# Performance work log

Measured on AMD Instinct MI355X. Metric: run time of the kernel, lower is better.

The kernel has to match this reference:

```python
import jax, jax.numpy as jnp
import numpy as np

N_NODES = 50000
N_EDGES = 800000
IN_CH, HID_CH, OUT_CH = 512, 256, 128


def setup_inputs() -> dict:
    key = jax.random.key(0)
    k = jax.random.split(key, 6)
    x = jax.random.normal(k[0], (N_NODES, IN_CH), dtype=jnp.float32)
    edge_index = jax.random.randint(k[1], (2, N_EDGES), 0, N_NODES, dtype=jnp.int64)
    # Glorot-ish scaled weights
    W0 = jax.random.normal(k[2], (IN_CH, HID_CH), dtype=jnp.float32) * (1.0 / np.sqrt(IN_CH))
    b0 = jnp.zeros((HID_CH,), dtype=jnp.float32)
    W1 = jax.random.normal(k[3], (HID_CH, OUT_CH), dtype=jnp.float32) * (1.0 / np.sqrt(HID_CH))
    b1 = jnp.zeros((OUT_CH,), dtype=jnp.float32)
    PW = jax.random.normal(k[4], (OUT_CH, OUT_CH), dtype=jnp.float32) * (1.0 / np.sqrt(OUT_CH))
    Pb = jnp.zeros((OUT_CH,), dtype=jnp.float32)
    return {"x": x, "edge_index": edge_index, "W0": W0, "b0": b0,
            "W1": W1, "b1": b1, "PW": PW, "Pb": Pb}


def reference(x, edge_index, W0, b0, W1, b1, PW, Pb):
    N = x.shape[0]
    # GCN normalization with added self-loops (edge_weight=None -> ones)
    loop = jnp.arange(N, dtype=edge_index.dtype)
    src = jnp.concatenate([edge_index[0], loop])  # [E+N]
    dst = jnp.concatenate([edge_index[1], loop])
    w = jnp.ones(src.shape[0], dtype=x.dtype)
    deg = jax.ops.segment_sum(w, dst, num_segments=N)  # in-degree incl. self-loop
    dinv = jnp.where(deg > 0, jax.lax.rsqrt(jnp.maximum(deg, 1e-12)), 0.0)
    norm = dinv[src] * dinv[dst]  # [E+N]

    def gcn_conv(h, W, b):
        hl = h @ W                               # [N, F_out] linear first (PyG GCNConv)
        msg = norm[:, None] * hl[src]            # gather + scale  [E+N, F_out]
        return jax.ops.segment_sum(msg, dst, num_segments=N) + b

    # eval mode: dropout is identity
    h = jax.nn.relu(gcn_conv(x, W0, b0))
    h = gcn_conv(h, W1, b1)                      # last layer: no relu
    p = h @ PW + Pb                              # PGE linear [N, OUT]
    vals = jnp.max(p, axis=0)                    # torch.max(dim=0) -> (values, indices)
    idx = jnp.argmax(p, axis=0)
    return (h, vals, idx)
```

## Files before the change

### kernel.cpp

```cpp
#include <hip/hip_runtime.h>
#include <stdint.h>

#define N_NODES 50000
#define N_EDGES 800000
#define IN_CH   512
#define HID_CH  256
#define OUT_CH  128
#define NPAD    50048
#define SLOT    96

#define NB_E   3125
#define NB2    391
#define AP     36

#define PBKT  NB_E
#define PW0B  (PBKT + 64)
#define PW1B  (PW0B + 16)
#define PPWB  (PW1B + 8)

typedef unsigned short ushort_t;
typedef __attribute__((ext_vector_type(8))) short    short8;
typedef __attribute__((ext_vector_type(4))) float    floatx4;
typedef __attribute__((ext_vector_type(4))) _Float16 half4v;
typedef __attribute__((ext_vector_type(2))) _Float16 half2v;

__device__ inline ushort_t f2bf(float x) {
    union { float f; unsigned u; } v; v.f = x;
    unsigned r = v.u + 0x7fffu + ((v.u >> 16) & 1u);
    return (ushort_t)(r >> 16);
}
__device__ inline float bf2f(ushort_t h) {
    union { unsigned u; float f; } v; v.u = ((unsigned)h) << 16;
    return v.f;
}
__device__ inline void gl_lds16(const void* g, void* l) {
    __builtin_amdgcn_global_load_lds((const __attribute__((address_space(1))) void*)g,
                                     (__attribute__((address_space(3))) void*)l, 16, 0, 0);
}

#define SWZ(r) ((((r) >> 1) & 3) << 3)

__device__ inline void conv_splitT8(const float* __restrict__ W,
                                    ushort_t* __restrict__ WhT,
                                    ushort_t* __restrict__ WlT,
                                    int K, int N, int base) {
    float4 v0 = *(const float4*)(W + base);
    float4 v1 = *(const float4*)(W + base + 4);
    float vv[8] = {v0.x, v0.y, v0.z, v0.w, v1.x, v1.y, v1.z, v1.w};
    #pragma unroll
    for (int j = 0; j < 8; ++j) {
        int g = base + j;
        int k = g / N, n = g - k * N;
        int ks = k ^ SWZ(n);
        ushort_t h = f2bf(vv[j]);
        WhT[(size_t)n * K + ks] = h;
        WlT[(size_t)n * K + ks] = f2bf(vv[j] - bf2f(h));
    }
}

__global__ __launch_bounds__(256) void k_prep(const int* __restrict__ esrc,
                                              const int* __restrict__ edst,
                                              const float* __restrict__ W0,
                                              const float* __restrict__ W1,
                                              const float* __restrict__ PW,
                                              int* __restrict__ cnt,
                                              int* __restrict__ slots,
                                              ushort_t* W0hT, ushort_t* W0lT,
                                              ushort_t* W1hT, ushort_t* W1lT,
                                              ushort_t* PWhT, ushort_t* PWlT) {
    int b = blockIdx.x, tid = threadIdx.x;
    if (b < PBKT) {
        int e = b * 256 + tid;
        if (e < N_EDGES) {
            int d = edst[e];
            int c = atomicAdd(&cnt[d], 1);
            slots[(size_t)d * SLOT + c] = esrc[e];
        }
    } else if (b < PW0B) {
        conv_splitT8(W0, W0hT, W0lT, IN_CH, HID_CH, (b - PBKT) * 2048 + tid * 8);
    } else if (b < PW1B) {
        conv_splitT8(W1, W1hT, W1lT, HID_CH, OUT_CH, (b - PW0B) * 2048 + tid * 8);
    } else {
        conv_splitT8(PW, PWhT, PWlT, OUT_CH, OUT_CH, (b - PW1B) * 2048 + tid * 8);
    }
}

__global__ __launch_bounds__(256) void k_dinv(const int* __restrict__ cnt,
                                              float* __restrict__ dinv) {
    int i = blockIdx.x * 256 + threadIdx.x;
    if (i < N_NODES) dinv[i] = rsqrtf((float)cnt[i] + 1.0f);
}

__global__ __launch_bounds__(256, 3) void gemm0_x(const float* __restrict__ A,
                                                  const ushort_t* __restrict__ BhT,
                                                  const ushort_t* __restrict__ BlT,
                                                  const float* __restrict__ dinv,
                                                  _Float16* __restrict__ C,
                                                  int M, int N) {
    constexpr int KT = IN_CH;
    constexpr int NT = KT / 32;
    __shared__ float    smA[128 * AP];
    __shared__ ushort_t smB[2][128 * 32];
    const int tid  = threadIdx.x;
    const int wave = tid >> 6, lane = tid & 63;
    const int m0 = blockIdx.y * 128, n0 = blockIdx.x * 128;

    const float* psrc[5];
    float*       adst[5];
    #pragma unroll
    for (int i = 0; i < 5; ++i) {
        int c = wave + 4 * i;
        int cc = (c < 18) ? c : 0;
        int p = cc * 256 + lane * 4;
        int r = p / AP, col = p - r * AP;
        int gr = min(m0 + r, M - 1);
        int gc = (col < 32) ? col : 0;
        psrc[i] = A + (size_t)gr * KT + gc;
        adst[i] = smA + cc * 256;
    }

    const int c0 = wave * 128 + lane, c1 = c0 + 64;
    const ushort_t* gbh0 = BhT + (size_t)(n0 + (c0 >> 2)) * KT + (c0 & 3) * 8;
    const ushort_t* gbh1 = BhT + (size_t)(n0 + (c1 >> 2)) * KT + (c1 & 3) * 8;
    const ushort_t* gbl0 = BlT + (size_t)(n0 + (c0 >> 2)) * KT + (c0 & 3) * 8;
    const ushort_t* gbl1 = BlT + (size_t)(n0 + (c1 >> 2)) * KT + (c1 & 3) * 8;
    ushort_t* lb0 = &smB[0][wave * 1024];  ushort_t* lb1 = &smB[0][wave * 1024 + 512];
    ushort_t* lc0 = &smB[1][wave * 1024];  ushort_t* lc1 = &smB[1][wave * 1024 + 512];

    floatx4 zero = {0.f, 0.f, 0.f, 0.f};
    floatx4 acc[4][4];
    #pragma unroll
    for (int i = 0; i < 4; ++i)
        #pragma unroll
        for (int j = 0; j < 4; ++j) acc[i][j] = zero;

    const int wm = (wave & 1) * 64, wn = (wave >> 1) * 64;
    const int fr = lane & 15, fq = lane >> 4;
    const int sx = SWZ(fr);

    for (int t = 0; t < NT; ++t) {
        #pragma unroll
        for (int i = 0; i < 5; ++i)
            if (wave + 4 * i < 18) { gl_lds16(psrc[i], adst[i]); psrc[i] += 32; }
        gl_lds16(gbh0, lb0); gl_lds16(gbh1, lb1);
        gl_lds16(gbl0, lc0); gl_lds16(gbl1, lc1);
        gbh0 += 32; gbh1 += 32; gbl0 += 32; gbl1 += 32;
        __syncthreads();
        short8 afh[4], afl[4], bfh[4], bfl[4];
        #pragma unroll
        for (int tt = 0; tt < 4; ++tt) {
            const float* ap = &smA[(wm + tt * 16 + fr) * AP + fq * 8];
            float4 v0 = *(const float4*)ap;
            float4 v1 = *(const float4*)(ap + 4);
            float f[8] = {v0.x, v0.y, v0.z, v0.w, v1.x, v1.y, v1.z, v1.w};
            union { unsigned u[4]; short8 v; } hh, ll;
            #pragma unroll
            for (int j = 0; j < 4; ++j) {
                unsigned ua = __float_as_uint(f[2 * j]);
                unsigned ub = __float_as_uint(f[2 * j + 1]);
                unsigned ha = ua & 0xffff0000u, hb = ub & 0xffff0000u;
                hh.u[j] = (ha >> 16) | hb;
                float ra = f[2 * j]     - __uint_as_float(ha);
                float rb = f[2 * j + 1] - __uint_as_float(hb);
                ll.u[j] = (__float_as_uint(ra) >> 16) | (__float_as_uint(rb) & 0xffff0000u);
            }
            afh[tt] = hh.v; afl[tt] = ll.v;
            int bi = (wn + tt * 16 + fr) * 32 + (fq * 8 ^ sx);
            bfh[tt] = *(const short8*)&smB[0][bi];
            bfl[tt] = *(const short8*)&smB[1][bi];
        }
        #pragma unroll
        for (int i = 0; i < 4; ++i)
            #pragma unroll
            for (int j = 0; j < 4; ++j) {
                acc[i][j] = __builtin_amdgcn_mfma_f32_16x16x32_bf16(afh[i], bfh[j], acc[i][j], 0, 0, 0);
                acc[i][j] = __builtin_amdgcn_mfma_f32_16x16x32_bf16(afh[i], bfl[j], acc[i][j], 0, 0, 0);
                acc[i][j] = __builtin_amdgcn_mfma_f32_16x16x32_bf16(afl[i], bfh[j], acc[i][j], 0, 0, 0);
            }
        __syncthreads();
    }
    const int colb = n0 + wn + fr;
    #pragma unroll
    for (int i = 0; i < 4; ++i) {
        int rowb = m0 + wm + i * 16 + fq * 4;
        #pragma unroll
        for (int r = 0; r < 4; ++r) {
            int row = rowb + r;
            if (row < M) {
                float dv = dinv[row];
                _Float16* cp = C + (size_t)row * N + colb;
                cp[0]  = (_Float16)(acc[i][0][r] * dv);
                cp[16] = (_Float16)(acc[i][1][r] * dv);
                cp[32] = (_Float16)(acc[i][2][r] * dv);
                cp[48] = (_Float16)(acc[i][3][r] * dv);
            }
        }
    }
}

template <int KT>
__global__ __launch_bounds__(256) void gemm_bf(const ushort_t* __restrict__ Ah,
                                               const ushort_t* __restrict__ Al,
                                               const ushort_t* __restrict__ BhT,
                                               const ushort_t* __restrict__ BlT,
                                               const float* __restrict__ dinv,
                                               _Float16* __restrict__ C,
                                               int M, int N) {
    constexpr int NT = KT / 32;
    __shared__ ushort_t sm[4][128 * 32];
    const int tid  = threadIdx.x;
    const int wave = tid >> 6, lane = tid & 63;
    const int m0 = blockIdx.y * 128, n0 = blockIdx.x * 128;

    const int c0 = wave * 128 + lane, c1 = c0 + 64;
    const int ar0 = min(m0 + (c0 >> 2), M - 1), ar1 = min(m0 + (c1 >> 2), M - 1);
    const ushort_t* gah0 = Ah + (size_t)ar0 * KT + (c0 & 3) * 8;
    const ushort_t* gah1 = Ah + (size_t)ar1 * KT + (c1 & 3) * 8;
    const ushort_t* gal0 = Al + (size_t)ar0 * KT + (c0 & 3) * 8;
    const ushort_t* gal1 = Al + (size_t)ar1 * KT + (c1 & 3) * 8;
    const ushort_t* gbh0 = BhT + (size_t)(n0 + (c0 >> 2)) * KT + (c0 & 3) * 8;
    const ushort_t* gbh1 = BhT + (size_t)(n0 + (c1 >> 2)) * KT + (c1 & 3) * 8;
    const ushort_t* gbl0 = BlT + (size_t)(n0 + (c0 >> 2)) * KT + (c0 & 3) * 8;
    const ushort_t* gbl1 = BlT + (size_t)(n0 + (c1 >> 2)) * KT + (c1 & 3) * 8;
    ushort_t* la0 = &sm[0][wave * 1024];       ushort_t* la1 = &sm[0][wave * 1024 + 512];
    ushort_t* ll0 = &sm[1][wave * 1024];       ushort_t* ll1 = &sm[1][wave * 1024 + 512];
    ushort_t* lb0 = &sm[2][wave * 1024];       ushort_t* lb1 = &sm[2][wave * 1024 + 512];
    ushort_t* lc0 = &sm[3][wave * 1024];       ushort_t* lc1 = &sm[3][wave * 1024 + 512];

    floatx4 zero = {0.f, 0.f, 0.f, 0.f};
    floatx4 acc[4][4];
    #pragma unroll
    for (int i = 0; i < 4; ++i)
        #pragma unroll
        for (int j = 0; j < 4; ++j) acc[i][j] = zero;

    const int wm = (wave & 1) * 64, wn = (wave >> 1) * 64;
    const int fr = lane & 15, fq = lane >> 4;
    const int sx = SWZ(fr);

    for (int t = 0; t < NT; ++t) {
        gl_lds16(gah0, la0); gl_lds16(gah1, la1);
        gl_lds16(gal0, ll0); gl_lds16(gal1, ll1);
        gl_lds16(gbh0, lb0); gl_lds16(gbh1, lb1);
        gl_lds16(gbl0, lc0); gl_lds16(gbl1, lc1);
        gah0 += 32; gah1 += 32; gal0 += 32; gal1 += 32;
        gbh0 += 32; gbh1 += 32; gbl0 += 32; gbl1 += 32;
        __syncthreads();
        short8 afh[4], afl[4], bfh[4], bfl[4];
        #pragma unroll
        for (int tt = 0; tt < 4; ++tt) {
            int ai = (wm + tt * 16 + fr) * 32 + (fq * 8 ^ sx);
            int bi = (wn + tt * 16 + fr) * 32 + (fq * 8 ^ sx);
            afh[tt] = *(const short8*)&sm[0][ai];
            afl[tt] = *(const short8*)&sm[1][ai];
            bfh[tt] = *(const short8*)&sm[2][bi];
            bfl[tt] = *(const short8*)&sm[3][bi];
        }
        #pragma unroll
        for (int i = 0; i < 4; ++i)
            #pragma unroll
            for (int j = 0; j < 4; ++j) {
                acc[i][j] = __builtin_amdgcn_mfma_f32_16x16x32_bf16(afh[i], bfh[j], acc[i][j], 0, 0, 0);
                acc[i][j] = __builtin_amdgcn_mfma_f32_16x16x32_bf16(afh[i], bfl[j], acc[i][j], 0, 0, 0);
                acc[i][j] = __builtin_amdgcn_mfma_f32_16x16x32_bf16(afl[i], bfh[j], acc[i][j], 0, 0, 0);
            }
        __syncthreads();
    }
    const int colb = n0 + wn + fr;
    #pragma unroll
    for (int i = 0; i < 4; ++i) {
        int rowb = m0 + wm + i * 16 + fq * 4;
        #pragma unroll
        for (int r = 0; r < 4; ++r) {
            int row = rowb + r;
            if (row < M) {
                float dv = dinv[row];
                _Float16* cp = C + (size_t)row * N + colb;
                cp[0]  = (_Float16)(acc[i][0][r] * dv);
                cp[16] = (_Float16)(acc[i][1][r] * dv);
                cp[32] = (_Float16)(acc[i][2][r] * dv);
                cp[48] = (_Float16)(acc[i][3][r] * dv);
            }
        }
    }
}

__global__ __launch_bounds__(256) void gemm_pge(const ushort_t* __restrict__ Ah,
                                                const ushort_t* __restrict__ Al,
                                                const ushort_t* __restrict__ BhT,
                                                const ushort_t* __restrict__ BlT,
                                                float* __restrict__ pv,
                                                int* __restrict__ pi,
                                                int M) {
    constexpr int KT = OUT_CH;
    constexpr int NT = KT / 32;
    __shared__ ushort_t sm[4][128 * 32];
    __shared__ float redv[8][128];
    __shared__ int   redi[8][128];
    const int tid  = threadIdx.x;
    const int wave = tid >> 6, lane = tid & 63;
    const int m0 = blockIdx.x * 128;

    const int c0 = wave * 128 + lane, c1 = c0 + 64;
    const int ar0 = min(m0 + (c0 >> 2), M - 1), ar1 = min(m0 + (c1 >> 2), M - 1);
    const ushort_t* gah0 = Ah + (size_t)ar0 * KT + (c0 & 3) * 8;
    const ushort_t* gah1 = Ah + (size_t)ar1 * KT + (c1 & 3) * 8;
    const ushort_t* gal0 = Al + (size_t)ar0 * KT + (c0 & 3) * 8;
    const ushort_t* gal1 = Al + (size_t)ar1 * KT + (c1 & 3) * 8;
    const ushort_t* gbh0 = BhT + (size_t)(c0 >> 2) * KT + (c0 & 3) * 8;
    const ushort_t* gbh1 = BhT + (size_t)(c1 >> 2) * KT + (c1 & 3) * 8;
    const ushort_t* gbl0 = BlT + (size_t)(c0 >> 2) * KT + (c0 & 3) * 8;
    const ushort_t* gbl1 = BlT + (size_t)(c1 >> 2) * KT + (c1 & 3) * 8;
    ushort_t* la0 = &sm[0][wave * 1024];       ushort_t* la1 = &sm[0][wave * 1024 + 512];
    ushort_t* ll0 = &sm[1][wave * 1024];       ushort_t* ll1 = &sm[1][wave * 1024 + 512];
    ushort_t* lb0 = &sm[2][wave * 1024];       ushort_t* lb1 = &sm[2][wave * 1024 + 512];
    ushort_t* lc0 = &sm[3][wave * 1024];       ushort_t* lc1 = &sm[3][wave * 1024 + 512];

    floatx4 zero = {0.f, 0.f, 0.f, 0.f};
    floatx4 acc[4][4];
    #pragma unroll
    for (int i = 0; i < 4; ++i)
        #pragma unroll
        for (int j = 0; j < 4; ++j) acc[i][j] = zero;

    const int wm = (wave & 1) * 64, wn = (wave >> 1) * 64;
    const int fr = lane & 15, fq = lane >> 4;
    const int sx = SWZ(fr);

    for (int t = 0; t < NT; ++t) {
        gl_lds16(gah0, la0); gl_lds16(gah1, la1);
        gl_lds16(gal0, ll0); gl_lds16(gal1, ll1);
        gl_lds16(gbh0, lb0); gl_lds16(gbh1, lb1);
        gl_lds16(gbl0, lc0); gl_lds16(gbl1, lc1);
        gah0 += 32; gah1 += 32; gal0 += 32; gal1 += 32;
        gbh0 += 32; gbh1 += 32; gbl0 += 32; gbl1 += 32;
        __syncthreads();
        short8 afh[4], afl[4], bfh[4], bfl[4];
        #pragma unroll
        for (int tt = 0; tt < 4; ++tt) {
            int ai = (wm + tt * 16 + fr) * 32 + (fq * 8 ^ sx);
            int bi = (wn + tt * 16 + fr) * 32 + (fq * 8 ^ sx);
            afh[tt] = *(const short8*)&sm[0][ai];
            afl[tt] = *(const short8*)&sm[1][ai];
            bfh[tt] = *(const short8*)&sm[2][bi];
            bfl[tt] = *(const short8*)&sm[3][bi];
        }
        #pragma unroll
        for (int i = 0; i < 4; ++i)
            #pragma unroll
            for (int j = 0; j < 4; ++j) {
                acc[i][j] = __builtin_amdgcn_mfma_f32_16x16x32_bf16(afh[i], bfh[j], acc[i][j], 0, 0, 0);
                acc[i][j] = __builtin_amdgcn_mfma_f32_16x16x32_bf16(afh[i], bfl[j], acc[i][j], 0, 0, 0);
                acc[i][j] = __builtin_amdgcn_mfma_f32_16x16x32_bf16(afl[i], bfh[j], acc[i][j], 0, 0, 0);
            }
        __syncthreads();
    }
    const int slot = (wave & 1) * 4 + fq;
    #pragma unroll
    for (int j = 0; j < 4; ++j) {
        float bv = -3.402823466e+38f; int bidx = 0;
        #pragma unroll
        for (int i = 0; i < 4; ++i) {
            int rowb = m0 + wm + i * 16 + fq * 4;
            #pragma unroll
            for (int r = 0; r < 4; ++r) {
                int row = rowb + r;
                float v = acc[i][j][r];
                if (row < M && v > bv) { bv = v; bidx = row; }
            }
        }
        redv[slot][wn + j * 16 + fr] = bv;
        redi[slot][wn + j * 16 + fr] = bidx;
    }
    __syncthreads();
    if (tid < 128) {
        float bv = redv[0][tid]; int bidx = redi[0][tid];
        #pragma unroll
        for (int s = 1; s < 8; ++s) {
            float v = redv[s][tid]; int ix = redi[s][tid];
            if (v > bv || (v == bv && ix < bidx)) { bv = v; bidx = ix; }
        }
        pv[blockIdx.x * 128 + tid] = bv;
        pi[blockIdx.x * 128 + tid] = bidx;
    }
}

__global__ __launch_bounds__(128) void agg256_relu_bf(const _Float16* __restrict__ hl,
                                                      const float* __restrict__ dinv,
                                                      const int* __restrict__ cnt,
                                                      const int* __restrict__ slots,
                                                      const float* __restrict__ bias,
                                                      ushort_t* __restrict__ oh,
                                                      ushort_t* __restrict__ ol) {
    int d = blockIdx.x * 2 + (threadIdx.x >> 6);
    int lane = threadIdx.x & 63;
    float di = dinv[d];
    half4v v = ((const half4v*)(hl + (size_t)d * 256))[lane];
    float ax = (float)v[0], ay = (float)v[1], az = (float)v[2], aw = (float)v[3];
    const int* sl = slots + (size_t)d * SLOT;
    int n = cnt[d];
    for (int e = 0; e < n; e += 8) {
        int s[8]; float m[8]; half4v u[8];
        #pragma unroll
        for (int j = 0; j < 8; ++j) {
            bool live = (e + j) < n;
            s[j] = live ? sl[e + j] : d;
            m[j] = live ? 1.0f : 0.0f;
        }
        #pragma unroll
        for (int j = 0; j < 8; ++j) u[j] = ((const half4v*)(hl + (size_t)s[j] * 256))[lane];
        #pragma unroll
        for (int j = 0; j < 8; ++j) {
            ax += m[j] * (float)u[j][0]; ay += m[j] * (float)u[j][1];
            az += m[j] * (float)u[j][2]; aw += m[j] * (float)u[j][3];
        }
    }
    float4 b = ((const float4*)bias)[lane];
    float rx = fmaxf(fmaf(di, ax, b.x), 0.0f), ry = fmaxf(fmaf(di, ay, b.y), 0.0f);
    float rz = fmaxf(fmaf(di, az, b.z), 0.0f), rw = fmaxf(fmaf(di, aw, b.w), 0.0f);
    ushort4 hv, lv;
    hv.x = f2bf(rx); lv.x = f2bf(rx - bf2f(hv.x));
    hv.y = f2bf(ry); lv.y = f2bf(ry - bf2f(hv.y));
    hv.z = f2bf(rz); lv.z = f2bf(rz - bf2f(hv.z));
    hv.w = f2bf(rw); lv.w = f2bf(rw - bf2f(hv.w));
    int sidx = (lane * 4) ^ SWZ(d);
    *(ushort4*)&oh[(size_t)d * 256 + sidx] = hv;
    *(ushort4*)&ol[(size_t)d * 256 + sidx] = lv;
}

__global__ __launch_bounds__(128) void agg128_bias_bf(const _Float16* __restrict__ hl,
                                                      const float* __restrict__ dinv,
                                                      const int* __restrict__ cnt,
                                                      const int* __restrict__ slots,
                                                      const float* __restrict__ bias,
                                                      float* __restrict__ out,
                                                      ushort_t* __restrict__ oh,
                                                      ushort_t* __restrict__ ol) {
    int d = blockIdx.x * 2 + (threadIdx.x >> 6);
    int lane = threadIdx.x & 63;
    float di = dinv[d];
    half2v v = ((const half2v*)(hl + (size_t)d * 128))[lane];
    float ax = (float)v[0], ay = (float)v[1];
    const int* sl = slots + (size_t)d * SLOT;
    int n = cnt[d];
    for (int e = 0; e < n; e += 8) {
        int s[8]; float m[8]; half2v u[8];
        #pragma unroll
        for (int j = 0; j < 8; ++j) {
            bool live = (e + j) < n;
            s[j] = live ? sl[e + j] : d;
            m[j] = live ? 1.0f : 0.0f;
        }
        #pragma unroll
        for (int j = 0; j < 8; ++j) u[j] = ((const half2v*)(hl + (size_t)s[j] * 128))[lane];
        #pragma unroll
        for (int j = 0; j < 8; ++j) { ax += m[j] * (float)u[j][0]; ay += m[j] * (float)u[j][1]; }
    }
    float2 b = ((const float2*)bias)[lane];
    float rx = fmaf(di, ax, b.x), ry = fmaf(di, ay, b.y);
    ((float2*)(out + (size_t)d * 128))[lane] = make_float2(rx, ry);
    ushort2 hv, lv;
    hv.x = f2bf(rx); lv.x = f2bf(rx - bf2f(hv.x));
    hv.y = f2bf(ry); lv.y = f2bf(ry - bf2f(hv.y));
    int sidx = (lane * 2) ^ SWZ(d);
    *(ushort2*)&oh[(size_t)d * 128 + sidx] = hv;
    *(ushort2*)&ol[(size_t)d * 128 + sidx] = lv;
}

__global__ __launch_bounds__(256) void k_reduce2(const float* __restrict__ pv,
                                                 const int* __restrict__ pi,
                                                 const float* __restrict__ Pb,
                                                 float* __restrict__ out) {
    int c = threadIdx.x & 127, sub = threadIdx.x >> 7;
    float best = -3.402823466e+38f;
    int bi = 0;
    for (int b = sub; b < NB2; b += 2) {
        float v = pv[b * 128 + c];
        int ix = pi[b * 128 + c];
        if (v > best || (v == best && ix < bi)) { best = v; bi = ix; }
    }
    __shared__ float sv[128];
    __shared__ int   si[128];
    if (sub == 1) { sv[c] = best; si[c] = bi; }
    __syncthreads();
    if (sub == 0) {
        float v1 = sv[c]; int i1 = si[c];
        if (v1 > best || (v1 == best && i1 < bi)) { best = v1; bi = i1; }
        out[(size_t)N_NODES * OUT_CH + c]       = best + Pb[c];
        out[(size_t)N_NODES * OUT_CH + 128 + c] = (float)bi;
    }
}

extern "C" void kernel_launch(void* const* d_in, const int* in_sizes, int n_in,
                              void* d_out, int out_size, void* d_ws, size_t ws_size,
                              hipStream_t stream) {
    const float* x  = (const float*)d_in[0];
    const int*   ei = (const int*)d_in[1];
    const float* W0 = (const float*)d_in[2];
    const float* b0 = (const float*)d_in[3];
    const float* W1 = (const float*)d_in[4];
    const float* b1 = (const float*)d_in[5];
    const float* PW = (const float*)d_in[6];
    const float* Pb = (const float*)d_in[7];
    float* out = (float*)d_out;
    const int* esrc = ei;
    const int* edst = ei + N_EDGES;

    char* w = (char*)d_ws;
    size_t off = 0;
    auto alloc = [&](size_t bytes) -> void* {
        void* p = (void*)(w + off);
        off = (off + bytes + 255) & ~(size_t)255;
        return p;
    };
    int*       cnt    = (int*)alloc((size_t)N_NODES * 4);
    float*     dinv   = (float*)alloc((size_t)N_NODES * 4);
    int*       slots  = (int*)alloc((size_t)N_NODES * SLOT * 4);
    float*     pmax_v = (float*)alloc((size_t)NB2 * 128 * 4);
    int*       pmax_i = (int*)alloc((size_t)NB2 * 128 * 4);
    _Float16*  bufH   = (_Float16*)alloc((size_t)NPAD * 256 * 2);
    ushort_t*  h0h    = (ushort_t*)alloc((size_t)N_NODES * HID_CH * 2);
    ushort_t*  h0l    = (ushort_t*)alloc((size_t)N_NODES * HID_CH * 2);
    ushort_t*  h1h    = (ushort_t*)alloc((size_t)N_NODES * OUT_CH * 2);
    ushort_t*  h1l    = (ushort_t*)alloc((size_t)N_NODES * OUT_CH * 2);
    ushort_t*  W0hT   = (ushort_t*)alloc((size_t)IN_CH * HID_CH * 2);
    ushort_t*  W0lT   = (ushort_t*)alloc((size_t)IN_CH * HID_CH * 2);
    ushort_t*  W1hT   = (ushort_t*)alloc((size_t)HID_CH * OUT_CH * 2);
    ushort_t*  W1lT   = (ushort_t*)alloc((size_t)HID_CH * OUT_CH * 2);
    ushort_t*  PWhT   = (ushort_t*)alloc((size_t)OUT_CH * OUT_CH * 2);
    ushort_t*  PWlT   = (ushort_t*)alloc((size_t)OUT_CH * OUT_CH * 2);

    hipMemsetAsync(cnt, 0, (size_t)N_NODES * 4, stream);
    k_prep<<<PPWB, 256, 0, stream>>>(esrc, edst, W0, W1, PW, cnt, slots,
                                     W0hT, W0lT, W1hT, W1lT, PWhT, PWlT);
    k_dinv<<<196, 256, 0, stream>>>(cnt, dinv);

    gemm0_x<<<dim3(HID_CH / 128, NB2), 256, 0, stream>>>(
        x, W0hT, W0lT, dinv, bufH, N_NODES, HID_CH);
    agg256_relu_bf<<<N_NODES / 2, 128, 0, stream>>>(bufH, dinv, cnt, slots, b0, h0h, h0l);

    gemm_bf<HID_CH><<<dim3(1, NB2), 256, 0, stream>>>(
        h0h, h0l, W1hT, W1lT, dinv, bufH, N_NODES, OUT_CH);
    agg128_bias_bf<<<N_NODES / 2, 128, 0, stream>>>(bufH, dinv, cnt, slots, b1,
                                                    out, h1h, h1l);

    gemm_pge<<<NB2, 256, 0, stream>>>(h1h, h1l, PWhT, PWlT, pmax_v, pmax_i, N_NODES);
    k_reduce2<<<1, 256, 0, stream>>>(pmax_v, pmax_i, Pb, out);

    (void)in_sizes; (void)n_in; (void)out_size; (void)ws_size;
}
```

Measured before the change: 452.8 us.

## Convert A to split-bf16 once in LDS, prefetch next tile, inline dinv

The first GEMM now loads x tiles into registers, splits them into bf16 hi/lo once, and stores them swizzled in LDS. The next tile is prefetched during compute using explicit waitcnt and barriers, so each wave no longer redoes the conversion on its own LDS reads. The separate dinv kernel is removed and rsqrt(cnt+1) is computed inline in the GEMM epilogues and aggregation kernels. Aggregation gathers unroll to 16 and the GEMMs get an occupancy hint of 4. The hand-placed waitcnt counts are fragile and raise register pressure.

```diff
diff --git a/kernel.cpp b/kernel.cpp
--- a/kernel.cpp
+++ b/kernel.cpp
@@ -11,7 +11,6 @@
 
 #define NB_E   3125
 #define NB2    391
-#define AP     36
 
 #define PBKT  NB_E
 #define PW0B  (PBKT + 64)
@@ -85,39 +84,25 @@
     }
 }
 
-__global__ __launch_bounds__(256) void k_dinv(const int* __restrict__ cnt,
-                                              float* __restrict__ dinv) {
-    int i = blockIdx.x * 256 + threadIdx.x;
-    if (i < N_NODES) dinv[i] = rsqrtf((float)cnt[i] + 1.0f);
-}
-
-__global__ __launch_bounds__(256, 3) void gemm0_x(const float* __restrict__ A,
+__global__ __launch_bounds__(256, 4) void gemm0_x(const float* __restrict__ A,
                                                   const ushort_t* __restrict__ BhT,
                                                   const ushort_t* __restrict__ BlT,
-                                                  const float* __restrict__ dinv,
+                                                  const int* __restrict__ cnt,
                                                   _Float16* __restrict__ C,
                                                   int M, int N) {
     constexpr int KT = IN_CH;
     constexpr int NT = KT / 32;
-    __shared__ float    smA[128 * AP];
+    __shared__ ushort_t smA[2][128 * 32];
     __shared__ ushort_t smB[2][128 * 32];
     const int tid  = threadIdx.x;
     const int wave = tid >> 6, lane = tid & 63;
     const int m0 = blockIdx.y * 128, n0 = blockIdx.x * 128;
 
-    const float* psrc[5];
-    float*       adst[5];
-    #pragma unroll
-    for (int i = 0; i < 5; ++i) {
-        int c = wave + 4 * i;
-        int cc = (c < 18) ? c : 0;
-        int p = cc * 256 + lane * 4;
-        int r = p / AP, col = p - r * AP;
-        int gr = min(m0 + r, M - 1);
-        int gc = (col < 32) ? col : 0;
-        psrc[i] = A + (size_t)gr * KT + gc;
-        adst[i] = smA + cc * 256;
-    }
+    const int sr = tid >> 1, sseg = tid & 1;
+    const float* gA = A + (size_t)min(m0 + sr, M - 1) * KT + sseg * 16;
+    const int swa = (sr >> 1) & 3;
+    const int wo0 = sr * 32 + (((sseg * 2)     ^ swa) * 8);
+    const int wo1 = sr * 32 + (((sseg * 2 + 1) ^ swa) * 8);
 
     const int c0 = wave * 128 + lane, c1 = c0 + 64;
     const ushort_t* gbh0 = BhT + (size_t)(n0 + (c0 >> 2)) * KT + (c0 & 3) * 8;
@@ -127,6 +112,32 @@
     ushort_t* lb0 = &smB[0][wave * 1024];  ushort_t* lb1 = &smB[0][wave * 1024 + 512];
     ushort_t* lc0 = &smB[1][wave * 1024];  ushort_t* lc1 = &smB[1][wave * 1024 + 512];
 
+    float4 q0, q1, q2, q3;
+    auto loadA = [&]() {
+        q0 = ((const float4*)gA)[0]; q1 = ((const float4*)gA)[1];
+        q2 = ((const float4*)gA)[2]; q3 = ((const float4*)gA)[3];
+        gA += 32;
+    };
+    auto writeA = [&]() {
+        float vv[16] = {q0.x, q0.y, q0.z, q0.w, q1.x, q1.y, q1.z, q1.w,
+                        q2.x, q2.y, q2.z, q2.w, q3.x, q3.y, q3.z, q3.w};
+        unsigned hp[8], lp[8];
+        #pragma unroll
+        for (int j = 0; j < 8; ++j) {
+            unsigned ua = __float_as_uint(vv[2 * j]);
+            unsigned ub = __float_as_uint(vv[2 * j + 1]);
+            unsigned ha = ua & 0xffff0000u, hb = ub & 0xffff0000u;
+            hp[j] = (ua >> 16) | hb;
+            float ra = vv[2 * j]     - __uint_as_float(ha);
+            float rb = vv[2 * j + 1] - __uint_as_float(hb);
+            lp[j] = (__float_as_uint(ra) >> 16) | (__float_as_uint(rb) & 0xffff0000u);
+        }
+        *(uint4*)&smA[0][wo0] = make_uint4(hp[0], hp[1], hp[2], hp[3]);
+        *(uint4*)&smA[0][wo1] = make_uint4(hp[4], hp[5], hp[6], hp[7]);
+        *(uint4*)&smA[1][wo0] = make_uint4(lp[0], lp[1], lp[2], lp[3]);
+        *(uint4*)&smA[1][wo1] = make_uint4(lp[4], lp[5], lp[6], lp[7]);
+    };
+
     floatx4 zero = {0.f, 0.f, 0.f, 0.f};
     floatx4 acc[4][4];
     #pragma unroll
@@ -138,34 +149,31 @@
     const int fr = lane & 15, fq = lane >> 4;
     const int sx = SWZ(fr);
 
+    loadA();
     for (int t = 0; t < NT; ++t) {
-        #pragma unroll
-        for (int i = 0; i < 5; ++i)
-            if (wave + 4 * i < 18) { gl_lds16(psrc[i], adst[i]); psrc[i] += 32; }
         gl_lds16(gbh0, lb0); gl_lds16(gbh1, lb1);
         gl_lds16(gbl0, lc0); gl_lds16(gbl1, lc1);
         gbh0 += 32; gbh1 += 32; gbl0 += 32; gbl1 += 32;
-        __syncthreads();
+        writeA();
+        __builtin_amdgcn_sched_barrier(0);
+        if (t + 1 < NT) {
+            loadA();
+            __builtin_amdgcn_sched_barrier(0);
+            asm volatile("s_waitcnt vmcnt(4) lgkmcnt(0)" ::: "memory");
+        } else {
+            asm volatile("s_waitcnt vmcnt(0) lgkmcnt(0)" ::: "memory");
+        }
+        __builtin_amdgcn_sched_barrier(0);
+        __builtin_amdgcn_s_barrier();
+        __builtin_amdgcn_sched_barrier(0);
+
         short8 afh[4], afl[4], bfh[4], bfl[4];
         #pragma unroll
         for (int tt = 0; tt < 4; ++tt) {
-            const float* ap = &smA[(wm + tt * 16 + fr) * AP + fq * 8];
-            float4 v0 = *(const float4*)ap;
-            float4 v1 = *(const float4*)(ap + 4);
-            float f[8] = {v0.x, v0.y, v0.z, v0.w, v1.x, v1.y, v1.z, v1.w};
-            union { unsigned u[4]; short8 v; } hh, ll;
-            #pragma unroll
-            for (int j = 0; j < 4; ++j) {
-                unsigned ua = __float_as_uint(f[2 * j]);
-                unsigned ub = __float_as_uint(f[2 * j + 1]);
-                unsigned ha = ua & 0xffff0000u, hb = ub & 0xffff0000u;
-                hh.u[j] = (ha >> 16) | hb;
-                float ra = f[2 * j]     - __uint_as_float(ha);
-                float rb = f[2 * j + 1] - __uint_as_float(hb);
-                ll.u[j] = (__float_as_uint(ra) >> 16) | (__float_as_uint(rb) & 0xffff0000u);
-            }
-            afh[tt] = hh.v; afl[tt] = ll.v;
+            int ai = (wm + tt * 16 + fr) * 32 + (fq * 8 ^ sx);
             int bi = (wn + tt * 16 + fr) * 32 + (fq * 8 ^ sx);
+            afh[tt] = *(const short8*)&smA[0][ai];
+            afl[tt] = *(const short8*)&smA[1][ai];
             bfh[tt] = *(const short8*)&smB[0][bi];
             bfl[tt] = *(const short8*)&smB[1][bi];
         }
@@ -177,7 +185,9 @@
                 acc[i][j] = __builtin_amdgcn_mfma_f32_16x16x32_bf16(afh[i], bfl[j], acc[i][j], 0, 0, 0);
                 acc[i][j] = __builtin_amdgcn_mfma_f32_16x16x32_bf16(afl[i], bfh[j], acc[i][j], 0, 0, 0);
             }
-        __syncthreads();
+        __builtin_amdgcn_sched_barrier(0);
+        __builtin_amdgcn_s_barrier();
+        __builtin_amdgcn_sched_barrier(0);
     }
     const int colb = n0 + wn + fr;
     #pragma unroll
@@ -187,7 +197,7 @@
         for (int r = 0; r < 4; ++r) {
             int row = rowb + r;
             if (row < M) {
-                float dv = dinv[row];
+                float dv = rsqrtf((float)cnt[row] + 1.0f);
                 _Float16* cp = C + (size_t)row * N + colb;
                 cp[0]  = (_Float16)(acc[i][0][r] * dv);
                 cp[16] = (_Float16)(acc[i][1][r] * dv);
@@ -199,13 +209,13 @@
 }
 
 template <int KT>
-__global__ __launch_bounds__(256) void gemm_bf(const ushort_t* __restrict__ Ah,
-                                               const ushort_t* __restrict__ Al,
-                                               const ushort_t* __restrict__ BhT,
-                                               const ushort_t* __restrict__ BlT,
-                                               const float* __restrict__ dinv,
-                                               _Float16* __restrict__ C,
-                                               int M, int N) {
+__global__ __launch_bounds__(256, 4) void gemm_bf(const ushort_t* __restrict__ Ah,
+                                                  const ushort_t* __restrict__ Al,
+                                                  const ushort_t* __restrict__ BhT,
+                                                  const ushort_t* __restrict__ BlT,
+                                                  const int* __restrict__ cnt,
+                                                  _Float16* __restrict__ C,
+                                                  int M, int N) {
     constexpr int NT = KT / 32;
     __shared__ ushort_t sm[4][128 * 32];
     const int tid  = threadIdx.x;
@@ -274,7 +284,7 @@
         for (int r = 0; r < 4; ++r) {
             int row = rowb + r;
             if (row < M) {
-                float dv = dinv[row];
+                float dv = rsqrtf((float)cnt[row] + 1.0f);
                 _Float16* cp = C + (size_t)row * N + colb;
                 cp[0]  = (_Float16)(acc[i][0][r] * dv);
                 cp[16] = (_Float16)(acc[i][1][r] * dv);
@@ -386,7 +396,6 @@
 }
 
 __global__ __launch_bounds__(128) void agg256_relu_bf(const _Float16* __restrict__ hl,
-                                                      const float* __restrict__ dinv,
                                                       const int* __restrict__ cnt,
                                                       const int* __restrict__ slots,
                                                       const float* __restrict__ bias,
@@ -394,23 +403,23 @@
                                                       ushort_t* __restrict__ ol) {
     int d = blockIdx.x * 2 + (threadIdx.x >> 6);
     int lane = threadIdx.x & 63;
-    float di = dinv[d];
+    int n = cnt[d];
+    float di = rsqrtf((float)n + 1.0f);
     half4v v = ((const half4v*)(hl + (size_t)d * 256))[lane];
     float ax = (float)v[0], ay = (float)v[1], az = (float)v[2], aw = (float)v[3];
     const int* sl = slots + (size_t)d * SLOT;
-    int n = cnt[d];
-    for (int e = 0; e < n; e += 8) {
-        int s[8]; float m[8]; half4v u[8];
-        #pragma unroll
-        for (int j = 0; j < 8; ++j) {
+    for (int e = 0; e < n; e += 16) {
+        int s[16]; float m[16]; half4v u[16];
+        #pragma unroll
+        for (int j = 0; j < 16; ++j) {
             bool live = (e + j) < n;
             s[j] = live ? sl[e + j] : d;
             m[j] = live ? 1.0f : 0.0f;
         }
         #pragma unroll
-        for (int j = 0; j < 8; ++j) u[j] = ((const half4v*)(hl + (size_t)s[j] * 256))[lane];
-        #pragma unroll
-        for (int j = 0; j < 8; ++j) {
+        for (int j = 0; j < 16; ++j) u[j] = ((const half4v*)(hl + (size_t)s[j] * 256))[lane];
+        #pragma unroll
+        for (int j = 0; j < 16; ++j) {
             ax += m[j] * (float)u[j][0]; ay += m[j] * (float)u[j][1];
             az += m[j] * (float)u[j][2]; aw += m[j] * (float)u[j][3];
         }
@@ -429,7 +438,6 @@
 }
 
 __global__ __launch_bounds__(128) void agg128_bias_bf(const _Float16* __restrict__ hl,
-                                                      const float* __restrict__ dinv,
                                                       const int* __restrict__ cnt,
                                                       const int* __restrict__ slots,
                                                       const float* __restrict__ bias,
@@ -438,23 +446,23 @@
                                                       ushort_t* __restrict__ ol) {
     int d = blockIdx.x * 2 + (threadIdx.x >> 6);
     int lane = threadIdx.x & 63;
-    float di = dinv[d];
+    int n = cnt[d];
+    float di = rsqrtf((float)n + 1.0f);
     half2v v = ((const half2v*)(hl + (size_t)d * 128))[lane];
     float ax = (float)v[0], ay = (float)v[1];
     const int* sl = slots + (size_t)d * SLOT;
-    int n = cnt[d];
-    for (int e = 0; e < n; e += 8) {
-        int s[8]; float m[8]; half2v u[8];
-        #pragma unroll
-        for (int j = 0; j < 8; ++j) {
+    for (int e = 0; e < n; e += 16) {
+        int s[16]; float m[16]; half2v u[16];
+        #pragma unroll
+        for (int j = 0; j < 16; ++j) {
             bool live = (e + j) < n;
             s[j] = live ? sl[e + j] : d;
             m[j] = live ? 1.0f : 0.0f;
         }
         #pragma unroll
-        for (int j = 0; j < 8; ++j) u[j] = ((const half2v*)(hl + (size_t)s[j] * 128))[lane];
-        #pragma unroll
-        for (int j = 0; j < 8; ++j) { ax += m[j] * (float)u[j][0]; ay += m[j] * (float)u[j][1]; }
+        for (int j = 0; j < 16; ++j) u[j] = ((const half2v*)(hl + (size_t)s[j] * 128))[lane];
+        #pragma unroll
+        for (int j = 0; j < 16; ++j) { ax += m[j] * (float)u[j][0]; ay += m[j] * (float)u[j][1]; }
     }
     float2 b = ((const float2*)bias)[lane];
     float rx = fmaf(di, ax, b.x), ry = fmaf(di, ay, b.y);
@@ -514,7 +522,6 @@
         return p;
     };
     int*       cnt    = (int*)alloc((size_t)N_NODES * 4);
-    float*     dinv   = (float*)alloc((size_t)N_NODES * 4);
     int*       slots  = (int*)alloc((size_t)N_NODES * SLOT * 4);
     float*     pmax_v = (float*)alloc((size_t)NB2 * 128 * 4);
     int*       pmax_i = (int*)alloc((size_t)NB2 * 128 * 4);
@@ -533,15 +540,14 @@
     hipMemsetAsync(cnt, 0, (size_t)N_NODES * 4, stream);
     k_prep<<<PPWB, 256, 0, stream>>>(esrc, edst, W0, W1, PW, cnt, slots,
                                      W0hT, W0lT, W1hT, W1lT, PWhT, PWlT);
-    k_dinv<<<196, 256, 0, stream>>>(cnt, dinv);
 
     gemm0_x<<<dim3(HID_CH / 128, NB2), 256, 0, stream>>>(
-        x, W0hT, W0lT, dinv, bufH, N_NODES, HID_CH);
-    agg256_relu_bf<<<N_NODES / 2, 128, 0, stream>>>(bufH, dinv, cnt, slots, b0, h0h, h0l);
+        x, W0hT, W0lT, cnt, bufH, N_NODES, HID_CH);
+    agg256_relu_bf<<<N_NODES / 2, 128, 0, stream>>>(bufH, cnt, slots, b0, h0h, h0l);
 
     gemm_bf<HID_CH><<<dim3(1, NB2), 256, 0, stream>>>(
-        h0h, h0l, W1hT, W1lT, dinv, bufH, N_NODES, OUT_CH);
-    agg128_bias_bf<<<N_NODES / 2, 128, 0, stream>>>(bufH, dinv, cnt, slots, b1,
+        h0h, h0l, W1hT, W1lT, cnt, bufH, N_NODES, OUT_CH);
+    agg128_bias_bf<<<N_NODES / 2, 128, 0, stream>>>(bufH, cnt, slots, b1,
                                                     out, h1h, h1l);
 
     gemm_pge<<<NB2, 256, 0, stream>>>(h1h, h1l, PWhT, PWlT, pmax_v, pmax_i, N_NODES);
```

New measurement: 499.5 us. 1.1x slower.
